# Performance work log

Hardware: AMD Instinct MI355X
Metric: run time of the kernel (lower is better)

Reference implementation:

```python
import jax, jax.numpy as jnp
import numpy as np

B, S, D, H = 4, 2048, 1024, 16
DH = D // H  # 64
EPS = 1e-6


def _phi(t):
    # positive feature map used by linear attention: elu(x) + 1
    return jax.nn.elu(t) + 1.0


def setup_inputs() -> dict:
    key = jax.random.key(0)
    ks = jax.random.split(key, 5)
    scale = 1.0 / np.sqrt(D)
    return {
        "x": jax.random.normal(ks[0], (B, S, D), dtype=jnp.float32),
        "Wq": jax.random.normal(ks[1], (D, D), dtype=jnp.float32) * scale,
        "Wk": jax.random.normal(ks[2], (D, D), dtype=jnp.float32) * scale,
        "Wv": jax.random.normal(ks[3], (D, D), dtype=jnp.float32) * scale,
        "Wo": jax.random.normal(ks[4], (D, D), dtype=jnp.float32) * scale,
    }


def reference(x, Wq, Wk, Wv, Wo):
    b, s, d = x.shape
    # projections -> [b, s, H, DH]
    q = _phi((x @ Wq).reshape(b, s, H, DH))
    k = _phi((x @ Wk).reshape(b, s, H, DH))
    v = (x @ Wv).reshape(b, s, H, DH)

    # time-major for scan: [s, b, H, DH]
    qT = jnp.moveaxis(q, 1, 0)
    kT = jnp.moveaxis(k, 1, 0)
    vT = jnp.moveaxis(v, 1, 0)

    S0 = jnp.zeros((b, H, DH, DH), dtype=x.dtype)  # matrix memory per head
    z0 = jnp.zeros((b, H, DH), dtype=x.dtype)      # normalizer per head

    def step(carry, qkv):
        Smat, z = carry
        qt, kt, vt = qkv
        Smat = Smat + kt[..., :, None] * vt[..., None, :]  # [b,H,DH,DH]
        z = z + kt
        num = jnp.einsum('bhd,bhde->bhe', qt, Smat)
        den = jnp.einsum('bhd,bhd->bh', qt, z)
        out = num / (den[..., None] + EPS)
        return (Smat, z), out

    _, outs = jax.lax.scan(step, (S0, z0), (qT, kT, vT))  # [s,b,H,DH]
    out = jnp.moveaxis(outs, 0, 1).reshape(b, s, d)
    return out @ Wo
```

## Files before the change

kernel.cpp:

```cpp
#include <hip/hip_runtime.h>
#include <hip/hip_bf16.h>
#include <math.h>

constexpr int Bb  = 4;
constexpr int SEQ = 2048;
constexpr int Dd  = 1024;
constexpr int Hh  = 16;
constexpr int DHh = 64;
constexpr int Cc  = 64;
constexpr int NCc = SEQ / Cc;
constexpr int Mm  = Bb * SEQ;
constexpr float EPSf = 1e-6f;

typedef __attribute__((ext_vector_type(8))) short bf16x8;
typedef __attribute__((ext_vector_type(4))) float f32x4;
typedef __attribute__((ext_vector_type(8))) unsigned short u16x8;

__device__ __forceinline__ float bf2f(unsigned short u) {
    return __uint_as_float((unsigned)u << 16);
}
__device__ __forceinline__ unsigned short f2bf(float f) {
    unsigned u = __float_as_uint(f);
    unsigned r = u + 0x7fff + ((u >> 16) & 1);
    return (unsigned short)(r >> 16);
}
__device__ __forceinline__ int swz(int row, int col) {
    return col ^ (((row >> 3) & 7) << 3);
}

__global__ __launch_bounds__(256)
void prep(const float* __restrict__ x,
          const float* __restrict__ W0, const float* __restrict__ W1,
          const float* __restrict__ W2, const float* __restrict__ W3,
          unsigned short* __restrict__ xb, unsigned short* __restrict__ WT) {
    __shared__ float t[64][65];
    const int tid = threadIdx.x;
    if (blockIdx.x < 4096) {
        int i = blockIdx.x * 256 + tid;
        const float4* p = reinterpret_cast<const float4*>(x) + (size_t)i * 2;
        float4 a = p[0], b = p[1];
        u16x8 o;
        o[0] = f2bf(a.x); o[1] = f2bf(a.y); o[2] = f2bf(a.z); o[3] = f2bf(a.w);
        o[4] = f2bf(b.x); o[5] = f2bf(b.y); o[6] = f2bf(b.z); o[7] = f2bf(b.w);
        *(reinterpret_cast<u16x8*>(xb) + i) = o;
        return;
    }
    const int tb = blockIdx.x - 4096;
    const int z  = tb >> 8;
    const int by = (tb >> 4) & 15, bx = tb & 15;
    const float* W = (z == 0) ? W0 : (z == 1) ? W1 : (z == 2) ? W2 : W3;
    unsigned short* T = WT + (size_t)z * Dd * Dd;
    const int r0 = by * 64, c0 = bx * 64;
    const int lr = tid >> 4, lc4 = (tid & 15) * 4;
#pragma unroll
    for (int it = 0; it < 4; ++it) {
        int row = lr + it * 16;
        float4 v = *reinterpret_cast<const float4*>(W + (size_t)(r0 + row) * Dd + c0 + lc4);
        t[row][lc4 + 0] = v.x; t[row][lc4 + 1] = v.y;
        t[row][lc4 + 2] = v.z; t[row][lc4 + 3] = v.w;
    }
    __syncthreads();
#pragma unroll
    for (int it = 0; it < 4; ++it) {
        int col = lr + it * 16;
        ushort4 o;
        o.x = f2bf(t[lc4 + 0][col]); o.y = f2bf(t[lc4 + 1][col]);
        o.z = f2bf(t[lc4 + 2][col]); o.w = f2bf(t[lc4 + 3][col]);
        *reinterpret_cast<ushort4*>(T + (size_t)(c0 + col) * Dd + r0 + lc4) = o;
    }
}

template<int QKV>
__global__ __launch_bounds__(512, 1)
void gemm_pipe(const unsigned short* __restrict__ A, const unsigned short* __restrict__ BT,
               float* __restrict__ outF, unsigned short* __restrict__ oQ,
               unsigned short* __restrict__ oK, unsigned short* __restrict__ oV) {
    constexpr int Kd  = 1024;
    constexpr int BK  = 64;
    constexpr int NT  = Kd / BK;
    constexpr int GX  = QKV ? 12 : 4;
    constexpr int NWG = GX * 64;
    constexpr int BUFSZ = (128 + 256) * BK;

    __shared__ __align__(16) unsigned short lds[3 * BUFSZ];

    const int wg0 = blockIdx.x;
    const int wg  = (wg0 & 7) * (NWG >> 3) + (wg0 >> 3);
    const int by = wg & 63, bx = wg >> 6;
    const int row0 = by * 128;
    const int col0 = bx * 256;

    const int tid  = threadIdx.x;
    const int lane = tid & 63;
    const int wave = tid >> 6;
    const int wm = (wave >> 2) * 64;
    const int wn = (wave & 3) * 64;
    const int fr = lane & 15;
    const int hi = lane >> 4;

    f32x4 acc[4][4];
#pragma unroll
    for (int mf = 0; mf < 4; ++mf)
#pragma unroll
        for (int nf = 0; nf < 4; ++nf) acc[mf][nf] = (f32x4){0.f, 0.f, 0.f, 0.f};

    auto stage1 = [&](int sel, int kt, int l) {
        unsigned short* base = &lds[sel * BUFSZ];
        int seg = l * 512 + tid;
        if (l < 2) {
            int row = seg >> 3, sp = seg & 7;
            int gcol = kt + ((sp ^ (row & 7)) << 3);
            __builtin_amdgcn_global_load_lds(
                (const __attribute__((address_space(1))) void*)(A + (size_t)(row0 + row) * Kd + gcol),
                (__attribute__((address_space(3))) void*)(base + seg * 8), 16, 0, 0);
        } else {
            int bseg = seg - 1024;
            int row = bseg >> 3, sp = bseg & 7;
            int gcol = kt + ((sp ^ (row & 7)) << 3);
            __builtin_amdgcn_global_load_lds(
                (const __attribute__((address_space(1))) void*)(BT + (size_t)(col0 + row) * Kd + gcol),
                (__attribute__((address_space(3))) void*)(base + 8192 + bseg * 8), 16, 0, 0);
        }
    };
    auto lda = [&](const unsigned short* bufA, int mf, int ks) {
        int row = wm + mf * 16 + fr;
        int sp = ((ks << 2) | hi) ^ (row & 7);
        return *reinterpret_cast<const bf16x8*>(bufA + row * 64 + sp * 8);
    };
    auto ldb = [&](const unsigned short* bufB, int nf, int ks) {
        int row = wn + nf * 16 + fr;
        int sp = ((ks << 2) | hi) ^ (row & 7);
        return *reinterpret_cast<const bf16x8*>(bufB + row * 64 + sp * 8);
    };

#pragma unroll
    for (int l = 0; l < 6; ++l) stage1(0, 0, l);
#pragma unroll
    for (int l = 0; l < 6; ++l) stage1(1, BK, l);

    int selc = 0;
    for (int t = 0; t < NT; ++t) {
        if (t < NT - 1) { asm volatile("s_waitcnt vmcnt(6)" ::: "memory"); }
        else            { asm volatile("s_waitcnt vmcnt(0)" ::: "memory"); }
        __builtin_amdgcn_sched_barrier(0);
        __builtin_amdgcn_s_barrier();
        __builtin_amdgcn_sched_barrier(0);

        const unsigned short* bufA = &lds[selc * BUFSZ];
        const unsigned short* bufB = bufA + 8192;
        int sels = selc + 2; if (sels >= 3) sels -= 3;
        const bool st = (t + 2 < NT);
        const int kt2 = (t + 2) * BK;

        bf16x8 a0_[4], a1_[4], bL[2], bM[2], bN[2], bO[2];

#pragma unroll
        for (int mf = 0; mf < 4; ++mf) a0_[mf] = lda(bufA, mf, 0);
        bL[0] = ldb(bufB, 0, 0); bL[1] = ldb(bufB, 1, 0);
        bM[0] = ldb(bufB, 2, 0); bM[1] = ldb(bufB, 3, 0);

        asm volatile("s_waitcnt lgkmcnt(2)" ::: "memory");
        __builtin_amdgcn_sched_barrier(0);
        __builtin_amdgcn_s_setprio(1);
#pragma unroll
        for (int mf = 0; mf < 4; ++mf) {
            acc[mf][0] = __builtin_amdgcn_mfma_f32_16x16x32_bf16(a0_[mf], bL[0], acc[mf][0], 0, 0, 0);
            acc[mf][1] = __builtin_amdgcn_mfma_f32_16x16x32_bf16(a0_[mf], bL[1], acc[mf][1], 0, 0, 0);
        }
        __builtin_amdgcn_s_setprio(0);

#pragma unroll
        for (int mf = 0; mf < 4; ++mf) a1_[mf] = lda(bufA, mf, 1);
        bN[0] = ldb(bufB, 0, 1); bN[1] = ldb(bufB, 1, 1);
        if (st) { stage1(sels, kt2, 0); stage1(sels, kt2, 1); stage1(sels, kt2, 2); }

        asm volatile("s_waitcnt lgkmcnt(6)" ::: "memory");
        __builtin_amdgcn_sched_barrier(0);
        __builtin_amdgcn_s_setprio(1);
#pragma unroll
        for (int mf = 0; mf < 4; ++mf) {
            acc[mf][2] = __builtin_amdgcn_mfma_f32_16x16x32_bf16(a0_[mf], bM[0], acc[mf][2], 0, 0, 0);
            acc[mf][3] = __builtin_amdgcn_mfma_f32_16x16x32_bf16(a0_[mf], bM[1], acc[mf][3], 0, 0, 0);
        }
        __builtin_amdgcn_s_setprio(0);

        bO[0] = ldb(bufB, 2, 1); bO[1] = ldb(bufB, 3, 1);
        if (st) { stage1(sels, kt2, 3); stage1(sels, kt2, 4); stage1(sels, kt2, 5); }

        asm volatile("s_waitcnt lgkmcnt(2)" ::: "memory");
        __builtin_amdgcn_sched_barrier(0);
        __builtin_amdgcn_s_setprio(1);
#pragma unroll
        for (int mf = 0; mf < 4; ++mf) {
            acc[mf][0] = __builtin_amdgcn_mfma_f32_16x16x32_bf16(a1_[mf], bN[0], acc[mf][0], 0, 0, 0);
            acc[mf][1] = __builtin_amdgcn_mfma_f32_16x16x32_bf16(a1_[mf], bN[1], acc[mf][1], 0, 0, 0);
        }
        __builtin_amdgcn_s_setprio(0);

        asm volatile("s_waitcnt lgkmcnt(0)" ::: "memory");
        __builtin_amdgcn_sched_barrier(0);
        __builtin_amdgcn_s_setprio(1);
#pragma unroll
        for (int mf = 0; mf < 4; ++mf) {
            acc[mf][2] = __builtin_amdgcn_mfma_f32_16x16x32_bf16(a1_[mf], bO[0], acc[mf][2], 0, 0, 0);
            acc[mf][3] = __builtin_amdgcn_mfma_f32_16x16x32_bf16(a1_[mf], bO[1], acc[mf][3], 0, 0, 0);
        }
        __builtin_amdgcn_s_setprio(0);

        selc = (selc == 2) ? 0 : selc + 1;
    }

    if (QKV) {
        const int sel = col0 >> 10;
        unsigned short* ob = (sel == 0) ? oQ : (sel == 1) ? oK : oV;
        const bool phi = (sel < 2);
        const int ncol0 = col0 & 1023;
#pragma unroll
        for (int mf = 0; mf < 4; ++mf)
#pragma unroll
            for (int nf = 0; nf < 4; ++nf)
#pragma unroll
                for (int r = 0; r < 4; ++r) {
                    int orow = row0 + wm + mf * 16 + hi * 4 + r;
                    int ocol = ncol0 + wn + nf * 16 + fr;
                    float v = acc[mf][nf][r];
                    if (phi) v = (v > 0.f) ? (v + 1.f) : __expf(v);
                    ob[(size_t)orow * Dd + ocol] = f2bf(v);
                }
    } else {
#pragma unroll
        for (int mf = 0; mf < 4; ++mf)
#pragma unroll
            for (int nf = 0; nf < 4; ++nf)
#pragma unroll
                for (int r = 0; r < 4; ++r) {
                    int orow = row0 + wm + mf * 16 + hi * 4 + r;
                    int ocol = col0 + wn + nf * 16 + fr;
                    outF[(size_t)orow * Dd + ocol] = acc[mf][nf][r];
                }
    }
}

__global__ __launch_bounds__(256)
void chunk_sums_mfma(const unsigned short* __restrict__ Kb, const unsigned short* __restrict__ Vb,
                     unsigned short* __restrict__ CSb, float* __restrict__ CZ) {
    const int blk = blockIdx.x;
    const int c  = blk & (NCc - 1);
    const int bh = blk >> 5;
    const int b  = bh >> 4;
    const int h  = bh & 15;
    const int tid  = threadIdx.x;
    const int wave = tid >> 6, lane = tid & 63;
    const int lo = lane & 15, hi = lane >> 4;
    const int wr = (wave >> 1) * 32, wc = (wave & 1) * 32;

    __shared__ __align__(16) unsigned short Kt[64][72];
    __shared__ __align__(16) unsigned short Vt[64][72];

    const size_t rowbase = ((size_t)b * SEQ + c * Cc) * Dd + (size_t)h * DHh;

#pragma unroll
    for (int it = 0; it < 2; ++it) {
        int idx = tid + it * 256;
        int r = idx >> 3, c8 = (idx & 7) * 8;
        u16x8 kv = *reinterpret_cast<const u16x8*>(Kb + rowbase + (size_t)r * Dd + c8);
        u16x8 vv = *reinterpret_cast<const u16x8*>(Vb + rowbase + (size_t)r * Dd + c8);
#pragma unroll
        for (int q = 0; q < 8; ++q) {
            int d = c8 + q;
            int sc = swz(d, r);
            Kt[d][sc] = kv[q];
            Vt[d][sc] = vv[q];
        }
    }
    __syncthreads();

    f32x4 acc[2][2];
#pragma unroll
    for (int mf = 0; mf < 2; ++mf)
#pragma unroll
        for (int nf = 0; nf < 2; ++nf) acc[mf][nf] = (f32x4){0.f, 0.f, 0.f, 0.f};

#pragma unroll
    for (int kb = 0; kb < 2; ++kb) {
        const int ko = kb * 32 + hi * 8;
        bf16x8 av[2], bk[2];
#pragma unroll
        for (int mf = 0; mf < 2; ++mf) {
            int row = wr + mf * 16 + lo;
            av[mf] = *reinterpret_cast<const bf16x8*>(&Vt[row][swz(row, ko)]);
        }
#pragma unroll
        for (int nf = 0; nf < 2; ++nf) {
            int row = wc + nf * 16 + lo;
            bk[nf] = *reinterpret_cast<const bf16x8*>(&Kt[row][swz(row, ko)]);
        }
#pragma unroll
        for (int mf = 0; mf < 2; ++mf)
#pragma unroll
            for (int nf = 0; nf < 2; ++nf)
                acc[mf][nf] = __builtin_amdgcn_mfma_f32_16x16x32_bf16(av[mf], bk[nf], acc[mf][nf], 0, 0, 0);
    }

    if (tid < DHh) {
        float s = 0.f;
#pragma unroll
        for (int e8 = 0; e8 < 8; ++e8) {
            u16x8 k8 = *reinterpret_cast<const u16x8*>(&Kt[tid][e8 * 8]);
#pragma unroll
            for (int q = 0; q < 8; ++q) s += bf2f(k8[q]);
        }
        CZ[((size_t)bh * NCc + c) * DHh + tid] = s;
    }

    unsigned short* csb = CSb + ((size_t)bh * NCc + c) * (DHh * DHh);
#pragma unroll
    for (int mf = 0; mf < 2; ++mf)
#pragma unroll
        for (int nf = 0; nf < 2; ++nf)
#pragma unroll
            for (int r = 0; r < 4; ++r) {
                int e = wr + mf * 16 + hi * 4 + r;
                int d = wc + nf * 16 + lo;
                csb[e * DHh + d] = f2bf(acc[mf][nf][r]);
            }
}

__global__ __launch_bounds__(256)
void chunk_scan3(unsigned short* __restrict__ CSb, float* __restrict__ CZ) {
    const int bh = blockIdx.x >> 3;
    const int sl = blockIdx.x & 7;
    const int tid = threadIdx.x;
    const int pos = sl * 512 + tid * 2;
    unsigned* p0 = reinterpret_cast<unsigned*>(CSb + (size_t)bh * NCc * (DHh * DHh) + pos);

    unsigned v[NCc];
#pragma unroll
    for (int c = 0; c < NCc; ++c) v[c] = p0[c * 2048];

    const bool doz = (sl == 0) && (tid < DHh);
    float zv[NCc];
    const size_t zbase = (size_t)bh * NCc * DHh + tid;
    if (doz) {
#pragma unroll
        for (int c = 0; c < NCc; ++c) zv[c] = CZ[zbase + (size_t)c * DHh];
    }

    float a0 = 0.f, a1 = 0.f;
#pragma unroll
    for (int c = 0; c < NCc; ++c) {
        p0[c * 2048] = (unsigned)f2bf(a0) | ((unsigned)f2bf(a1) << 16);
        a0 += bf2f((unsigned short)(v[c] & 0xffff));
        a1 += bf2f((unsigned short)(v[c] >> 16));
    }
    if (doz) {
        float accz = 0.f;
#pragma unroll
        for (int c = 0; c < NCc; ++c) {
            CZ[zbase + (size_t)c * DHh] = accz;
            accz += zv[c];
        }
    }
}

__global__ __launch_bounds__(256)
void chunk_out_mfma(const unsigned short* __restrict__ Qb, const unsigned short* __restrict__ Kb,
                    const unsigned short* __restrict__ Vb, const unsigned short* __restrict__ CSb,
                    const float* __restrict__ CZ, unsigned short* __restrict__ Ob) {
    const int blk = blockIdx.x;
    const int c  = blk & (NCc - 1);
    const int bh = blk >> 5;
    const int b  = bh >> 4;
    const int h  = bh & 15;
    const int tid  = threadIdx.x;
    const int wave = tid >> 6, lane = tid & 63;
    const int lo = lane & 15, hi = lane >> 4;
    const int wr = (wave >> 1) * 32, wc = (wave & 1) * 32;

    __shared__ __align__(16) unsigned short Qs[64][72];
    __shared__ __align__(16) unsigned short KP[64][72];
    __shared__ __align__(16) unsigned short Ss[64][72];
    __shared__ __align__(16) unsigned short Vt[64][72];
    __shared__ float zsL[DHh];
    __shared__ float rowp[64][2];
    __shared__ float denL[64];

    const size_t rowbase = ((size_t)b * SEQ + c * Cc) * Dd + (size_t)h * DHh;
    const unsigned short* csb = CSb + ((size_t)bh * NCc + c) * (DHh * DHh);

#pragma unroll
    for (int it = 0; it < 2; ++it) {
        int idx = tid + it * 256;
        int r = idx >> 3, c8 = (idx & 7) * 8;
        u16x8 qv = *reinterpret_cast<const u16x8*>(Qb + rowbase + (size_t)r * Dd + c8);
        u16x8 kv = *reinterpret_cast<const u16x8*>(Kb + rowbase + (size_t)r * Dd + c8);
        u16x8 vv = *reinterpret_cast<const u16x8*>(Vb + rowbase + (size_t)r * Dd + c8);
        u16x8 sv = *reinterpret_cast<const u16x8*>(csb + idx * 8);
        *reinterpret_cast<u16x8*>(&Qs[r][c8]) = qv;
        *reinterpret_cast<u16x8*>(&KP[r][c8]) = kv;
        *reinterpret_cast<u16x8*>(&Ss[r][c8]) = sv;
#pragma unroll
        for (int q = 0; q < 8; ++q) {
            int d = c8 + q;
            Vt[d][swz(d, r)] = vv[q];
        }
    }
    if (tid < DHh) zsL[tid] = CZ[((size_t)bh * NCc + c) * DHh + tid];
    __syncthreads();

    f32x4 accs[2][2], accO[2][2];
#pragma unroll
    for (int mf = 0; mf < 2; ++mf)
#pragma unroll
        for (int nf = 0; nf < 2; ++nf) {
            accs[mf][nf] = (f32x4){0.f, 0.f, 0.f, 0.f};
            accO[mf][nf] = (f32x4){0.f, 0.f, 0.f, 0.f};
        }

#pragma unroll
    for (int kb = 0; kb < 2; ++kb) {
        const int ko = kb * 32 + hi * 8;
        bf16x8 aq[2], bk[2], bs[2];
#pragma unroll
        for (int mf = 0; mf < 2; ++mf)
            aq[mf] = *reinterpret_cast<const bf16x8*>(&Qs[wr + mf * 16 + lo][ko]);
#pragma unroll
        for (int nf = 0; nf < 2; ++nf) {
            bk[nf] = *reinterpret_cast<const bf16x8*>(&KP[wc + nf * 16 + lo][ko]);
            bs[nf] = *reinterpret_cast<const bf16x8*>(&Ss[wc + nf * 16 + lo][ko]);
        }
#pragma unroll
        for (int mf = 0; mf < 2; ++mf)
#pragma unroll
            for (int nf = 0; nf < 2; ++nf) {
                accs[mf][nf] = __builtin_amdgcn_mfma_f32_16x16x32_bf16(aq[mf], bk[nf], accs[mf][nf], 0, 0, 0);
                accO[mf][nf] = __builtin_amdgcn_mfma_f32_16x16x32_bf16(aq[mf], bs[nf], accO[mf][nf], 0, 0, 0);
            }
    }

#pragma unroll
    for (int mf = 0; mf < 2; ++mf)
#pragma unroll
        for (int r = 0; r < 4; ++r) {
            int i = wr + mf * 16 + hi * 4 + r;
            float s = 0.f;
#pragma unroll
            for (int nf = 0; nf < 2; ++nf) {
                int j = wc + nf * 16 + lo;
                float v = (j <= i) ? accs[mf][nf][r] : 0.f;
                accs[mf][nf][r] = v;
                s += v;
            }
            s += __shfl_xor(s, 1); s += __shfl_xor(s, 2);
            s += __shfl_xor(s, 4); s += __shfl_xor(s, 8);
            if (lo == 0) rowp[i][wave & 1] = s;
        }
    __syncthreads();

#pragma unroll
    for (int mf = 0; mf < 2; ++mf)
#pragma unroll
        for (int nf = 0; nf < 2; ++nf)
#pragma unroll
            for (int r = 0; r < 4; ++r)
                KP[wr + mf * 16 + hi * 4 + r][wc + nf * 16 + lo] = f2bf(accs[mf][nf][r]);
    if (tid < 64) {
        float d = 0.f;
#pragma unroll
        for (int e8 = 0; e8 < 8; ++e8) {
            u16x8 q8 = *reinterpret_cast<const u16x8*>(&Qs[tid][e8 * 8]);
#pragma unroll
            for (int q = 0; q < 8; ++q) d += bf2f(q8[q]) * zsL[e8 * 8 + q];
        }
        denL[tid] = d + rowp[tid][0] + rowp[tid][1] + EPSf;
    }
    __syncthreads();

#pragma unroll
    for (int kb = 0; kb < 2; ++kb) {
        const int ko = kb * 32 + hi * 8;
        bf16x8 ap[2], bv[2];
#pragma unroll
        for (int mf = 0; mf < 2; ++mf)
            ap[mf] = *reinterpret_cast<const bf16x8*>(&KP[wr + mf * 16 + lo][ko]);
#pragma unroll
        for (int nf = 0; nf < 2; ++nf) {
            int row = wc + nf * 16 + lo;
            bv[nf] = *reinterpret_cast<const bf16x8*>(&Vt[row][swz(row, ko)]);
        }
#pragma unroll
        for (int mf = 0; mf < 2; ++mf)
#pragma unroll
            for (int nf = 0; nf < 2; ++nf)
                accO[mf][nf] = __builtin_amdgcn_mfma_f32_16x16x32_bf16(ap[mf], bv[nf], accO[mf][nf], 0, 0, 0);
    }

#pragma unroll
    for (int mf = 0; mf < 2; ++mf)
#pragma unroll
        for (int r = 0; r < 4; ++r) {
            int i = wr + mf * 16 + hi * 4 + r;
            float inv = 1.0f / denL[i];
#pragma unroll
            for (int nf = 0; nf < 2; ++nf) {
                int e = wc + nf * 16 + lo;
                Ob[rowbase + (size_t)i * Dd + e] = f2bf(accO[mf][nf][r] * inv);
            }
        }
}

extern "C" void kernel_launch(void* const* d_in, const int* in_sizes, int n_in,
                              void* d_out, int out_size, void* d_ws, size_t ws_size,
                              hipStream_t stream) {
    const float* x  = (const float*)d_in[0];
    const float* Wq = (const float*)d_in[1];
    const float* Wk = (const float*)d_in[2];
    const float* Wv = (const float*)d_in[3];
    const float* Wo = (const float*)d_in[4];

    const size_t NMD = (size_t)Mm * Dd;
    const size_t NW  = (size_t)Dd * Dd;
    unsigned short* xb  = (unsigned short*)d_ws;
    unsigned short* WT  = xb + NMD;
    unsigned short* Qb  = WT + 4 * NW;
    unsigned short* Kb  = Qb + NMD;
    unsigned short* Vb  = Kb + NMD;
    unsigned short* Obf = Vb + NMD;
    unsigned short* CSb = Obf + NMD;
    float* CZ = (float*)(CSb + (size_t)Bb * Hh * NCc * DHh * DHh);

    prep<<<4096 + 1024, 256, 0, stream>>>(x, Wq, Wk, Wv, Wo, xb, WT);

    gemm_pipe<1><<<12 * 64, 512, 0, stream>>>(xb, WT, nullptr, Qb, Kb, Vb);

    chunk_sums_mfma<<<Bb * Hh * NCc, 256, 0, stream>>>(Kb, Vb, CSb, CZ);
    chunk_scan3<<<Bb * Hh * 8, 256, 0, stream>>>(CSb, CZ);
    chunk_out_mfma<<<Bb * Hh * NCc, 256, 0, stream>>>(Qb, Kb, Vb, CSb, CZ, Obf);

    gemm_pipe<0><<<4 * 64, 512, 0, stream>>>(Obf, WT + 3 * NW, (float*)d_out, nullptr, nullptr, nullptr);
}
```

Baseline: 127.5 us.

## Stage GEMM epilogue through LDS for vectorized stores and remap XCD tiles

```diff
diff --git a/kernel.cpp b/kernel.cpp
--- a/kernel.cpp
+++ b/kernel.cpp
@@ -79,14 +79,15 @@
     constexpr int BK  = 64;
     constexpr int NT  = Kd / BK;
     constexpr int GX  = QKV ? 12 : 4;
-    constexpr int NWG = GX * 64;
     constexpr int BUFSZ = (128 + 256) * BK;
 
     __shared__ __align__(16) unsigned short lds[3 * BUFSZ];
 
     const int wg0 = blockIdx.x;
-    const int wg  = (wg0 & 7) * (NWG >> 3) + (wg0 >> 3);
-    const int by = wg & 63, bx = wg >> 6;
+    const int xcd = wg0 & 7;
+    const int i   = wg0 >> 3;
+    const int by  = xcd * 8 + i / GX;
+    const int bx  = i % GX;
     const int row0 = by * 128;
     const int col0 = bx * 256;
 
@@ -210,34 +211,49 @@
         selc = (selc == 2) ? 0 : selc + 1;
     }
 
+    __syncthreads();
+
     if (QKV) {
         const int sel = col0 >> 10;
         unsigned short* ob = (sel == 0) ? oQ : (sel == 1) ? oK : oV;
         const bool phi = (sel < 2);
         const int ncol0 = col0 & 1023;
+        unsigned short* eb = lds + wave * 4096;
 #pragma unroll
         for (int mf = 0; mf < 4; ++mf)
 #pragma unroll
             for (int nf = 0; nf < 4; ++nf)
 #pragma unroll
                 for (int r = 0; r < 4; ++r) {
-                    int orow = row0 + wm + mf * 16 + hi * 4 + r;
-                    int ocol = ncol0 + wn + nf * 16 + fr;
                     float v = acc[mf][nf][r];
                     if (phi) v = (v > 0.f) ? (v + 1.f) : __expf(v);
-                    ob[(size_t)orow * Dd + ocol] = f2bf(v);
+                    eb[(mf * 16 + hi * 4 + r) * 64 + nf * 16 + fr] = f2bf(v);
                 }
+        asm volatile("s_waitcnt lgkmcnt(0)" ::: "memory");
+#pragma unroll
+        for (int rr = 0; rr < 8; ++rr) {
+            int row = rr * 8 + (lane >> 3);
+            int c8  = (lane & 7) * 8;
+            u16x8 vv = *reinterpret_cast<const u16x8*>(eb + row * 64 + c8);
+            *reinterpret_cast<u16x8*>(ob + (size_t)(row0 + wm + row) * Dd + ncol0 + wn + c8) = vv;
+        }
     } else {
+        float* ebf = reinterpret_cast<float*>(lds) + wave * 4096;
 #pragma unroll
         for (int mf = 0; mf < 4; ++mf)
 #pragma unroll
             for (int nf = 0; nf < 4; ++nf)
 #pragma unroll
-                for (int r = 0; r < 4; ++r) {
-                    int orow = row0 + wm + mf * 16 + hi * 4 + r;
-                    int ocol = col0 + wn + nf * 16 + fr;
-                    outF[(size_t)orow * Dd + ocol] = acc[mf][nf][r];
-                }
+                for (int r = 0; r < 4; ++r)
+                    ebf[(mf * 16 + hi * 4 + r) * 64 + nf * 16 + fr] = acc[mf][nf][r];
+        asm volatile("s_waitcnt lgkmcnt(0)" ::: "memory");
+#pragma unroll
+        for (int rr = 0; rr < 16; ++rr) {
+            int row = rr * 4 + (lane >> 4);
+            int c4  = (lane & 15) * 4;
+            float4 vv = *reinterpret_cast<const float4*>(ebf + row * 64 + c4);
+            *reinterpret_cast<float4*>(outF + (size_t)(row0 + wm + row) * Dd + col0 + wn + c4) = vv;
+        }
     }
 }
 
```

New measurement: 123.9 us (median of 3 runs). -2.8%, faster.
